# Performance work log

Hardware: AMD Instinct MI355X
Metric: run time of the kernel (lower is better)

## Reference

```python
import jax, jax.numpy as jnp
import numpy as np

N = 100000   # nodes
E = 1600000  # edges
D = 128      # d_model
FF = 512     # dim_feedforward
EPS = 1e-5


def setup_inputs() -> dict:
    key = jax.random.key(0)
    ks = jax.random.split(key, 12)
    x = jax.random.normal(ks[0], (N, D), dtype=jnp.float32)
    edge_index = jax.random.randint(ks[1], (2, E), 0, N, dtype=jnp.int64)
    edge_weight = jax.random.uniform(ks[2], (E,), dtype=jnp.float32)
    sD = 1.0 / np.sqrt(D)
    sFF = 1.0 / np.sqrt(FF)
    W = jax.random.normal(ks[3], (D, D), dtype=jnp.float32) * sD   # GCN weight
    b = jnp.zeros((D,), jnp.float32)                                # GCN bias
    gamma = jnp.ones((D,), jnp.float32)                             # shared batchnorm
    beta = jnp.zeros((D,), jnp.float32)
    W1 = jax.random.normal(ks[4], (D, FF), dtype=jnp.float32) * sD  # MLP lin1
    b1 = jnp.zeros((FF,), jnp.float32)
    W2 = jax.random.normal(ks[5], (FF, D), dtype=jnp.float32) * sFF # MLP lin2
    b2 = jnp.zeros((D,), jnp.float32)
    return {"x": x, "edge_index": edge_index, "edge_weight": edge_weight,
            "W": W, "b": b, "gamma": gamma, "beta": beta,
            "W1": W1, "b1": b1, "W2": W2, "b2": b2}


def gcn_conv(x, edge_index, edge_weight, W, b):
    # GCNConv with add_self_loops=True (self-loop weight 1) and symmetric norm.
    h = x @ W                                   # [N, D]
    src, dst = edge_index[0], edge_index[1]
    deg = jax.ops.segment_sum(edge_weight, dst, num_segments=N) + 1.0
    dinv = jnp.where(deg > 0, jax.lax.rsqrt(deg), 0.0)
    norm = dinv[src] * edge_weight * dinv[dst]  # [E]
    out = jax.ops.segment_sum(norm[:, None] * h[src], dst, num_segments=N)
    out = out + (dinv * dinv)[:, None] * h      # self-loop contribution
    return out + b


def batch_norm(x, gamma, beta):
    # training-mode BatchNorm1d over the node (batch) dimension
    mu = jnp.mean(x, axis=0)
    var = jnp.mean((x - mu) ** 2, axis=0)
    return gamma * (x - mu) * jax.lax.rsqrt(var + EPS) + beta


def reference(x, edge_index, edge_weight, W, b, gamma, beta, W1, b1, W2, b2):
    x1 = batch_norm(x + gcn_conv(x, edge_index, edge_weight, W, b), gamma, beta)
    x2 = jax.nn.relu(x1 @ W1 + b1) @ W2 + b2    # MLP d_model->dim_ff->d_model
    return batch_norm(x1 + x2, gamma, beta)
```

## Files before the change

### kernel.cpp

```cpp
#include <hip/hip_runtime.h>

#define NN 100000
#define EE 1600000
#define DD 128
#define FFD 512
#define EPSV 1e-5f

#define SCB 98

typedef __attribute__((ext_vector_type(8))) short bf16x8;
typedef __attribute__((ext_vector_type(4))) float f32x4;
typedef unsigned long long ull;

__device__ __forceinline__ ushort f2b(float f) {
    uint u = __float_as_uint(f);
    return (ushort)((u + 0x7FFF + ((u >> 16) & 1)) >> 16);
}
__device__ __forceinline__ float b2f(ushort u) {
    return __uint_as_float(((uint)u) << 16);
}


__global__ __launch_bounds__(256) void k_init(ull* pk, float* s1, float* s2) {
    int i = blockIdx.x * 256 + threadIdx.x;
    if (i < NN) pk[i] = 0ULL;
    if (blockIdx.x == 0) { s1[threadIdx.x] = 0.f; s2[threadIdx.x] = 0.f; }
}


__global__ __launch_bounds__(256) void k_edge_deg(const int* __restrict__ ei,
                                                  const float* __restrict__ ew,
                                                  ull* __restrict__ pk,
                                                  int* __restrict__ rank) {
    int e = blockIdx.x * 256 + threadIdx.x;
    if (e < EE) {
        int dst = ei[EE + e];
        uint fx = (uint)(ew[e] * 16777216.0f + 0.5f);
        ull old = atomicAdd(&pk[dst], (1ULL << 32) | (ull)fx);
        rank[e] = (int)(old >> 32);
    }
}


__global__ __launch_bounds__(256) void k_scan_part(const ull* __restrict__ pk,
                                                   int* __restrict__ cnt,
                                                   float* __restrict__ dinv,
                                                   int* __restrict__ bsum) {
    __shared__ int red[4];
    int b = blockIdx.x, t = threadIdx.x;
    int base = b * 1024 + t * 4;
    int s = 0;
#pragma unroll
    for (int j = 0; j < 4; ++j) {
        int i = base + j;
        if (i < NN) {
            ull v = pk[i];
            int c = (int)(v >> 32);
            cnt[i] = c;
            dinv[i] = rsqrtf(1.0f + (float)(uint)(v & 0xFFFFFFFFu) * (1.0f / 16777216.0f));
            s += c;
        }
    }
#pragma unroll
    for (int d = 1; d < 64; d <<= 1) s += __shfl_xor(s, d);
    if ((t & 63) == 0) red[t >> 6] = s;
    __syncthreads();
    if (t == 0) bsum[b] = red[0] + red[1] + red[2] + red[3];
}

__global__ __launch_bounds__(128) void k_scan_base(int* __restrict__ bsum,
                                                   int* __restrict__ bbase,
                                                   int* __restrict__ start) {
    if (threadIdx.x == 0) {
        int run = 0;
        for (int i = 0; i < SCB; ++i) { bbase[i] = run; run += bsum[i]; }
        start[NN] = run;
    }
}

__global__ __launch_bounds__(256) void k_scan_fin(const int* __restrict__ cnt,
                                                  const int* __restrict__ bbase,
                                                  int* __restrict__ start) {
    __shared__ int ts[256];
    int b = blockIdx.x, t = threadIdx.x;
    int base = b * 1024 + t * 4;
    int v[4];
    int s = 0;
#pragma unroll
    for (int j = 0; j < 4; ++j) {
        int i = base + j;
        v[j] = (i < NN) ? cnt[i] : 0;
        s += v[j];
    }
    ts[t] = s;
    __syncthreads();
    for (int d = 1; d < 256; d <<= 1) {
        int add = (t >= d) ? ts[t - d] : 0;
        __syncthreads();
        ts[t] += add;
        __syncthreads();
    }
    int run = bbase[b] + ts[t] - s;
#pragma unroll
    for (int j = 0; j < 4; ++j) {
        int i = base + j;
        if (i < NN) {
            start[i] = run;
            run += v[j];
        }
    }
}


__global__ __launch_bounds__(256) void k_fill(const int* __restrict__ ei,
                                              const float* __restrict__ ew,
                                              const float* __restrict__ dinv,
                                              const int* __restrict__ start,
                                              const int* __restrict__ rank,
                                              uint2* __restrict__ csr) {
    int e = blockIdx.x * 256 + threadIdx.x;
    if (e < EE) {
        int src = ei[e];
        int dst = ei[EE + e];
        float nrm = dinv[src] * ew[e] * dinv[dst];
        int pos = start[dst] + rank[e];
        csr[pos] = make_uint2((uint)src, __float_as_uint(nrm));
    }
}


__global__ __launch_bounds__(256) void k_wcvt(const float* __restrict__ W,
                                              const float* __restrict__ W1,
                                              const float* __restrict__ W2,
                                              ushort* __restrict__ WTb,
                                              ushort* __restrict__ W1Tb,
                                              ushort* __restrict__ W2Tb) {
    int i = blockIdx.x * 256 + threadIdx.x;
    if (i < 16384) {
        int n = i >> 7, k = i & 127;
        WTb[i] = f2b(W[k * 128 + n]);
    } else if (i < 16384 + 65536) {
        int j = i - 16384;
        int f = j >> 7, k = j & 127;
        W1Tb[j] = f2b(W1[k * 512 + f]);
    } else {
        int j = i - 16384 - 65536;
        int jj = j >> 9, f = j & 511;
        W2Tb[j] = f2b(W2[f * 128 + jj]);
    }
}


__global__ __launch_bounds__(256) void k_xb(const float* __restrict__ x,
                                            ushort* __restrict__ xb) {
    long i = (long)blockIdx.x * 256 + threadIdx.x;
    float4 v = ((const float4*)x)[i];
    ushort4 o;
    o.x = f2b(v.x); o.y = f2b(v.y); o.z = f2b(v.z); o.w = f2b(v.w);
    ((ushort4*)xb)[i] = o;
}


__global__ __launch_bounds__(256) void k_gather(const ushort* __restrict__ xb,
                                                const float* __restrict__ dinv,
                                                const int* __restrict__ start,
                                                const uint2* __restrict__ csr,
                                                ushort* __restrict__ aggx) {
    int t = threadIdx.x;
    int wv = t >> 6, l = t & 63;
    const uint* xbu = (const uint*)xb;
    uint* aggu = (uint*)aggx;

    for (int k = 0; k < 8; ++k) {
        int node = blockIdx.x * 32 + wv * 8 + k;
        int e0 = start[node], e1 = start[node + 1];
        float a0 = 0.f, a1 = 0.f;
        int i = e0;
        for (; i + 8 <= e1; i += 8) {
            uint2 rr[8];
            uint hh[8];
#pragma unroll
            for (int u = 0; u < 8; ++u) rr[u] = csr[i + u];
#pragma unroll
            for (int u = 0; u < 8; ++u) hh[u] = xbu[rr[u].x * 64 + l];
#pragma unroll
            for (int u = 0; u < 8; ++u) {
                float n = __uint_as_float(rr[u].y);
                a0 = fmaf(n, b2f((ushort)(hh[u] & 0xFFFF)), a0);
                a1 = fmaf(n, b2f((ushort)(hh[u] >> 16)), a1);
            }
        }
        if (i + 4 <= e1) {
            uint2 rr[4];
            uint hh[4];
#pragma unroll
            for (int u = 0; u < 4; ++u) rr[u] = csr[i + u];
#pragma unroll
            for (int u = 0; u < 4; ++u) hh[u] = xbu[rr[u].x * 64 + l];
#pragma unroll
            for (int u = 0; u < 4; ++u) {
                float n = __uint_as_float(rr[u].y);
                a0 = fmaf(n, b2f((ushort)(hh[u] & 0xFFFF)), a0);
                a1 = fmaf(n, b2f((ushort)(hh[u] >> 16)), a1);
            }
            i += 4;
        }
        for (; i < e1; ++i) {
            uint2 r0 = csr[i];
            uint h0 = xbu[r0.x * 64 + l];
            float n0 = __uint_as_float(r0.y);
            a0 = fmaf(n0, b2f((ushort)(h0 & 0xFFFF)), a0);
            a1 = fmaf(n0, b2f((ushort)(h0 >> 16)), a1);
        }
        float dv = dinv[node];
        float sl = dv * dv;
        uint hs = xbu[node * 64 + l];
        a0 = fmaf(sl, b2f((ushort)(hs & 0xFFFF)), a0);
        a1 = fmaf(sl, b2f((ushort)(hs >> 16)), a1);
        aggu[node * 64 + l] = (uint)f2b(a0) | ((uint)f2b(a1) << 16);
    }
}


__global__ __launch_bounds__(256) void k_conv(const float* __restrict__ x,
                                              const ushort* __restrict__ aggx,
                                              const ushort* __restrict__ WTb,
                                              const float* __restrict__ b,
                                              ushort* __restrict__ yb,
                                              float* __restrict__ stats1) {
    __shared__ __align__(16) ushort xt[64][136];
    __shared__ __align__(16) ushort wt[128][136];
    int t = threadIdx.x;
    int row0 = blockIdx.x * 64;

    for (int i = t; i < 2048; i += 256) {
        int r = i >> 4, c8 = (i & 15) << 3;
        *(uint4*)&wt[r][c8] = ((const uint4*)WTb)[i];
    }
    for (int i = t; i < 1024; i += 256) {
        int r = i >> 4, c8 = (i & 15) << 3;
        int gr = row0 + r;
        uint4 v = make_uint4(0u, 0u, 0u, 0u);
        if (gr < NN) v = ((const uint4*)aggx)[(long)gr * 16 + (i & 15)];
        *(uint4*)&xt[r][c8] = v;
    }
    __syncthreads();

    int wv = t >> 6, l = t & 63;
    int lr = l & 15, lg = l >> 4;
    int rw = wv & 1, jw = wv >> 1;

    f32x4 z4 = {0.f, 0.f, 0.f, 0.f};
    f32x4 acc[4][2];
#pragma unroll
    for (int jt = 0; jt < 4; ++jt)
#pragma unroll
        for (int rt = 0; rt < 2; ++rt) acc[jt][rt] = z4;

#pragma unroll
    for (int ks = 0; ks < 4; ++ks) {
        bf16x8 qR0 = *(const bf16x8*)&xt[rw * 32 + lr][ks * 32 + lg * 8];
        bf16x8 qR1 = *(const bf16x8*)&xt[rw * 32 + 16 + lr][ks * 32 + lg * 8];
#pragma unroll
        for (int jt = 0; jt < 4; ++jt) {
            bf16x8 pW = *(const bf16x8*)&wt[jw * 64 + jt * 16 + lr][ks * 32 + lg * 8];
            acc[jt][0] = __builtin_amdgcn_mfma_f32_16x16x32_bf16(pW, qR0, acc[jt][0], 0, 0, 0);
            acc[jt][1] = __builtin_amdgcn_mfma_f32_16x16x32_bf16(pW, qR1, acc[jt][1], 0, 0, 0);
        }
    }

    float sj[4][4], qj[4][4];
#pragma unroll
    for (int jt = 0; jt < 4; ++jt)
#pragma unroll
        for (int g = 0; g < 4; ++g) { sj[jt][g] = 0.f; qj[jt][g] = 0.f; }

#pragma unroll
    for (int jt = 0; jt < 4; ++jt) {
        int jb = jw * 64 + jt * 16 + lg * 4;
        float4 bv = *(const float4*)&b[jb];
#pragma unroll
        for (int rt = 0; rt < 2; ++rt) {
            int rloc = rw * 32 + rt * 16 + lr;
            int r = row0 + rloc;
            if (r < NN) {
                float4 xv = *(const float4*)&x[(long)r * 128 + jb];
                float z0 = xv.x + acc[jt][rt][0] + bv.x;
                float z1 = xv.y + acc[jt][rt][1] + bv.y;
                float z2 = xv.z + acc[jt][rt][2] + bv.z;
                float z3 = xv.w + acc[jt][rt][3] + bv.w;
                ushort4 o;
                o.x = f2b(z0); o.y = f2b(z1); o.z = f2b(z2); o.w = f2b(z3);
                *(ushort4*)&yb[(long)r * 128 + jb] = o;
                sj[jt][0] += z0; sj[jt][1] += z1; sj[jt][2] += z2; sj[jt][3] += z3;
                qj[jt][0] += z0 * z0; qj[jt][1] += z1 * z1; qj[jt][2] += z2 * z2; qj[jt][3] += z3 * z3;
            }
        }
    }
#pragma unroll
    for (int jt = 0; jt < 4; ++jt)
#pragma unroll
        for (int g = 0; g < 4; ++g) {
#pragma unroll
            for (int d = 1; d < 16; d <<= 1) {
                sj[jt][g] += __shfl_xor(sj[jt][g], d);
                qj[jt][g] += __shfl_xor(qj[jt][g], d);
            }
        }
    __syncthreads();
    float* redS = (float*)&xt[0][0];
    float* redQ = redS + 512;
    if (lr == 0) {
#pragma unroll
        for (int jt = 0; jt < 4; ++jt)
#pragma unroll
            for (int g = 0; g < 4; ++g) {
                int j = jw * 64 + jt * 16 + lg * 4 + g;
                redS[wv * 128 + j] = sj[jt][g];
                redQ[wv * 128 + j] = qj[jt][g];
            }
    }
    __syncthreads();
    if (t < 128) {
        int w0 = (t >> 6) * 2;
        atomicAdd(&stats1[t], redS[w0 * 128 + t] + redS[(w0 + 1) * 128 + t]);
        atomicAdd(&stats1[128 + t], redQ[w0 * 128 + t] + redQ[(w0 + 1) * 128 + t]);
    }
}


__global__ __launch_bounds__(128) void k_bn_fin(const float* __restrict__ stats,
                                                const float* __restrict__ gamma,
                                                const float* __restrict__ beta,
                                                float* __restrict__ ac) {
    int c = threadIdx.x;
    float mu = stats[c] * (1.0f / NN);
    float var = stats[128 + c] * (1.0f / NN) - mu * mu;
    float a = gamma[c] * rsqrtf(var + EPSV);
    ac[c] = a;
    ac[128 + c] = beta[c] - mu * a;
}

__global__ __launch_bounds__(256) void k_affine(float* __restrict__ v,
                                                const float* __restrict__ ac) {
    long i = (long)blockIdx.x * 256 + threadIdx.x;
    int c4i = (int)(i & 31);
    float4 a = ((const float4*)ac)[c4i];
    float4 cc = ((const float4*)(ac + 128))[c4i];
    float4 v4 = ((float4*)v)[i];
    v4.x = a.x * v4.x + cc.x;
    v4.y = a.y * v4.y + cc.y;
    v4.z = a.z * v4.z + cc.z;
    v4.w = a.w * v4.w + cc.w;
    ((float4*)v)[i] = v4;
}


#define SWZ16(row, kb) ((((kb) ^ ((row) & 15)) << 3))

__global__ __launch_bounds__(512, 4) void k_mlp(const ushort* __restrict__ yb,
                                                const float* __restrict__ ac1,
                                                const ushort* __restrict__ W1Tb,
                                                const float* __restrict__ b1,
                                                const ushort* __restrict__ W2Tb,
                                                const float* __restrict__ b2,
                                                float* __restrict__ out,
                                                float* __restrict__ stats2) {
    __shared__ __align__(16) ushort xt[64 * 128];
    __shared__ __align__(16) ushort ht[64 * 128];
    __shared__ __align__(16) ushort wc[128 * 128];
    int t = threadIdx.x;
    int row0 = blockIdx.x * 64;

    for (int i = t; i < 1024; i += 512) {
        int r = i >> 4, kb = i & 15;
        int gr = row0 + r;
        ushort4 y0 = make_ushort4(0, 0, 0, 0), y1 = make_ushort4(0, 0, 0, 0);
        if (gr < NN) {
            long base = (long)gr * 32 + kb * 2;
            y0 = ((const ushort4*)yb)[base];
            y1 = ((const ushort4*)yb)[base + 1];
        }
        float4 a0 = ((const float4*)ac1)[kb * 2];
        float4 a1 = ((const float4*)ac1)[kb * 2 + 1];
        float4 c0 = ((const float4*)(ac1 + 128))[kb * 2];
        float4 c1 = ((const float4*)(ac1 + 128))[kb * 2 + 1];
        ushort4 o0, o1;
        o0.x = f2b(a0.x * b2f(y0.x) + c0.x);
        o0.y = f2b(a0.y * b2f(y0.y) + c0.y);
        o0.z = f2b(a0.z * b2f(y0.z) + c0.z);
        o0.w = f2b(a0.w * b2f(y0.w) + c0.w);
        o1.x = f2b(a1.x * b2f(y1.x) + c1.x);
        o1.y = f2b(a1.y * b2f(y1.y) + c1.y);
        o1.z = f2b(a1.z * b2f(y1.z) + c1.z);
        o1.w = f2b(a1.w * b2f(y1.w) + c1.w);
        ushort* dst = &xt[r * 128 + SWZ16(r, kb)];
        *(ushort4*)dst = o0;
        *(ushort4*)(dst + 4) = o1;
    }

    int wv = t >> 6, l = t & 63;
    int lr = l & 15, lg = l >> 4;
    int rw = wv & 3, jw = wv >> 2;
    int xrow = rw * 16 + lr;

    f32x4 z4 = {0.f, 0.f, 0.f, 0.f};
    f32x4 acc[4];
#pragma unroll
    for (int jt = 0; jt < 4; ++jt) acc[jt] = z4;

    for (int ch = 0; ch < 4; ++ch) {
        __syncthreads();
        for (int i = t; i < 2048; i += 512) {
            int f = i >> 4, kb = i & 15;
            uint4 v = ((const uint4*)W1Tb)[(ch * 128 + f) * 16 + kb];
            *(uint4*)&wc[f * 128 + SWZ16(f, kb)] = v;
        }
        __syncthreads();

        f32x4 hacc[4];
#pragma unroll
        for (int ft = 0; ft < 4; ++ft) hacc[ft] = z4;
#pragma unroll
        for (int ks = 0; ks < 4; ++ks) {
            int kcol = ((ks * 4 + lg) ^ lr) << 3;
            bf16x8 aR = *(const bf16x8*)&xt[xrow * 128 + kcol];
#pragma unroll
            for (int ft = 0; ft < 4; ++ft) {
                int f = jw * 64 + ft * 16 + lr;
                bf16x8 bW = *(const bf16x8*)&wc[f * 128 + kcol];
                hacc[ft] = __builtin_amdgcn_mfma_f32_16x16x32_bf16(aR, bW, hacc[ft], 0, 0, 0);
            }
        }
#pragma unroll
        for (int ft = 0; ft < 4; ++ft) {
            int fcol = jw * 64 + ft * 16 + lr;
            float b1v = b1[ch * 128 + fcol];
            int kbf = fcol >> 3, wi = fcol & 7;
#pragma unroll
            for (int rg = 0; rg < 4; ++rg) {
                int hrow = rw * 16 + lg * 4 + rg;
                ht[hrow * 128 + ((kbf ^ (hrow & 15)) << 3) + wi] =
                    f2b(fmaxf(hacc[ft][rg] + b1v, 0.f));
            }
        }
        __syncthreads();

        for (int i = t; i < 2048; i += 512) {
            int j = i >> 4, kb = i & 15;
            uint4 v = ((const uint4*)W2Tb)[j * 64 + ch * 16 + kb];
            *(uint4*)&wc[j * 128 + SWZ16(j, kb)] = v;
        }
        __syncthreads();

#pragma unroll
        for (int ks = 0; ks < 4; ++ks) {
            int kcol = ((ks * 4 + lg) ^ lr) << 3;
            bf16x8 qR = *(const bf16x8*)&ht[xrow * 128 + kcol];
#pragma unroll
            for (int jt = 0; jt < 4; ++jt) {
                int j = jw * 64 + jt * 16 + lr;
                bf16x8 pW = *(const bf16x8*)&wc[j * 128 + kcol];
                acc[jt] = __builtin_amdgcn_mfma_f32_16x16x32_bf16(pW, qR, acc[jt], 0, 0, 0);
            }
        }
    }

    float sj[4][4], qj[4][4];
    int r = row0 + xrow;
#pragma unroll
    for (int jt = 0; jt < 4; ++jt) {
        int jb = jw * 64 + jt * 16 + lg * 4;
        float4 b2v = *(const float4*)&b2[jb];
        int kbj = jb >> 3, wj = jb & 7;
        ushort4 xv = *(const ushort4*)&xt[xrow * 128 + ((kbj ^ lr) << 3) + wj];
        float z0 = b2f(xv.x) + acc[jt][0] + b2v.x;
        float z1 = b2f(xv.y) + acc[jt][1] + b2v.y;
        float z2 = b2f(xv.z) + acc[jt][2] + b2v.z;
        float z3 = b2f(xv.w) + acc[jt][3] + b2v.w;
        if (r < NN) {
            *(float4*)&out[(long)r * 128 + jb] = make_float4(z0, z1, z2, z3);
            sj[jt][0] = z0; sj[jt][1] = z1; sj[jt][2] = z2; sj[jt][3] = z3;
            qj[jt][0] = z0 * z0; qj[jt][1] = z1 * z1; qj[jt][2] = z2 * z2; qj[jt][3] = z3 * z3;
        } else {
            sj[jt][0] = 0.f; sj[jt][1] = 0.f; sj[jt][2] = 0.f; sj[jt][3] = 0.f;
            qj[jt][0] = 0.f; qj[jt][1] = 0.f; qj[jt][2] = 0.f; qj[jt][3] = 0.f;
        }
    }
#pragma unroll
    for (int jt = 0; jt < 4; ++jt)
#pragma unroll
        for (int g = 0; g < 4; ++g) {
#pragma unroll
            for (int d = 1; d < 16; d <<= 1) {
                sj[jt][g] += __shfl_xor(sj[jt][g], d);
                qj[jt][g] += __shfl_xor(qj[jt][g], d);
            }
        }
    __syncthreads();
    float* redS = (float*)&ht[0];
    float* redQ = redS + 1024;
    if (lr == 0) {
#pragma unroll
        for (int jt = 0; jt < 4; ++jt)
#pragma unroll
            for (int g = 0; g < 4; ++g) {
                int j = jw * 64 + jt * 16 + lg * 4 + g;
                redS[wv * 128 + j] = sj[jt][g];
                redQ[wv * 128 + j] = qj[jt][g];
            }
    }
    __syncthreads();
    if (t < 128) {
        int h = t >> 6;
        float S = redS[(h * 4 + 0) * 128 + t] + redS[(h * 4 + 1) * 128 + t]
                + redS[(h * 4 + 2) * 128 + t] + redS[(h * 4 + 3) * 128 + t];
        float Q = redQ[(h * 4 + 0) * 128 + t] + redQ[(h * 4 + 1) * 128 + t]
                + redQ[(h * 4 + 2) * 128 + t] + redQ[(h * 4 + 3) * 128 + t];
        atomicAdd(&stats2[t], S);
        atomicAdd(&stats2[128 + t], Q);
    }
}


extern "C" void kernel_launch(void* const* d_in, const int* in_sizes, int n_in,
                              void* d_out, int out_size, void* d_ws, size_t ws_size,
                              hipStream_t stream) {
    const float* x     = (const float*)d_in[0];
    const int*   ei    = (const int*)d_in[1];
    const float* ew    = (const float*)d_in[2];
    const float* W     = (const float*)d_in[3];
    const float* b     = (const float*)d_in[4];
    const float* gamma = (const float*)d_in[5];
    const float* beta  = (const float*)d_in[6];
    const float* W1    = (const float*)d_in[7];
    const float* b1    = (const float*)d_in[8];
    const float* W2    = (const float*)d_in[9];
    const float* b2    = (const float*)d_in[10];
    float* out = (float*)d_out;
    float* ws  = (float*)d_ws;

    ull*   pk     = (ull*)ws;
    float* dinv   = ws + 2 * NN;
    float* stats1 = ws + 3 * NN;
    float* ac1    = stats1 + 256;
    float* stats2 = ac1 + 256;
    float* ac2    = stats2 + 256;
    ushort* xb    = (ushort*)(ws + 3 * NN + 1024);
    ushort* WTb   = xb + (long)NN * 128;
    ushort* W1Tb  = WTb + 16384;
    ushort* W2Tb  = W1Tb + 65536;
    float*  fend  = ws + 3 * NN + 1024 + (long)NN * 64 + 73728;
    int*   cnt    = (int*)fend;
    int*   start  = cnt + NN;
    int*   bsum   = start + NN + 1;
    int*   bbase  = bsum + SCB;
    uint2* csr    = (uint2*)(((uintptr_t)(bbase + SCB) + 7) & ~(uintptr_t)7);
    ushort* aggx  = (ushort*)(csr + EE);
    int*   rank   = (int*)aggx;
    ushort* yb    = xb;

    int nb = (NN + 63) / 64;

    k_init<<<(NN + 255) / 256, 256, 0, stream>>>(pk, stats1, stats2);
    k_edge_deg<<<EE / 256, 256, 0, stream>>>(ei, ew, pk, rank);
    k_scan_part<<<SCB, 256, 0, stream>>>(pk, cnt, dinv, bsum);
    k_scan_base<<<1, 128, 0, stream>>>(bsum, bbase, start);
    k_scan_fin<<<SCB, 256, 0, stream>>>(cnt, bbase, start);
    k_fill<<<EE / 256, 256, 0, stream>>>(ei, ew, dinv, start, rank, csr);
    k_wcvt<<<576, 256, 0, stream>>>(W, W1, W2, WTb, W1Tb, W2Tb);
    k_xb<<<(NN * 32) / 256, 256, 0, stream>>>(x, xb);
    k_gather<<<NN / 32, 256, 0, stream>>>(xb, dinv, start, csr, aggx);
    k_conv<<<nb, 256, 0, stream>>>(x, aggx, WTb, b, yb, stats1);
    k_bn_fin<<<1, 128, 0, stream>>>(stats1, gamma, beta, ac1);
    k_mlp<<<nb, 512, 0, stream>>>(yb, ac1, W1Tb, b1, W2Tb, b2, out, stats2);
    k_bn_fin<<<1, 128, 0, stream>>>(stats2, gamma, beta, ac2);
    k_affine<<<(NN * 32) / 256, 256, 0, stream>>>(out, ac2);
}
```

Baseline: 373.6 us.

## Read bf16 residual in conv epilogue and double MLP row tile to 128

The conv epilogue now reads the residual x from the bf16 copy (xb, aliased with yb) instead of fp32 x, halving that read and writing the result back in place. The MLP kernel moves to 1024-thread blocks covering 128 rows, so each staged W1/W2 chunk serves twice as many rows and the block count halves. The risks are lower occupancy from the larger shared memory (about 96 KB per block) and slightly lower residual precision from using bf16 x.

New measurement: 383.9 us. 1.03x slower.

```diff
diff --git a/kernel.cpp b/kernel.cpp
--- a/kernel.cpp
+++ b/kernel.cpp
@@ -222,11 +222,10 @@
 }
 
 
-__global__ __launch_bounds__(256) void k_conv(const float* __restrict__ x,
-                                              const ushort* __restrict__ aggx,
+__global__ __launch_bounds__(256) void k_conv(const ushort* __restrict__ aggx,
                                               const ushort* __restrict__ WTb,
                                               const float* __restrict__ b,
-                                              ushort* __restrict__ yb,
+                                              ushort* xyb,
                                               float* __restrict__ stats1) {
     __shared__ __align__(16) ushort xt[64][136];
     __shared__ __align__(16) ushort wt[128][136];
@@ -284,14 +283,14 @@
             int rloc = rw * 32 + rt * 16 + lr;
             int r = row0 + rloc;
             if (r < NN) {
-                float4 xv = *(const float4*)&x[(long)r * 128 + jb];
-                float z0 = xv.x + acc[jt][rt][0] + bv.x;
-                float z1 = xv.y + acc[jt][rt][1] + bv.y;
-                float z2 = xv.z + acc[jt][rt][2] + bv.z;
-                float z3 = xv.w + acc[jt][rt][3] + bv.w;
+                ushort4 xv = *(const ushort4*)&xyb[(long)r * 128 + jb];
+                float z0 = b2f(xv.x) + acc[jt][rt][0] + bv.x;
+                float z1 = b2f(xv.y) + acc[jt][rt][1] + bv.y;
+                float z2 = b2f(xv.z) + acc[jt][rt][2] + bv.z;
+                float z3 = b2f(xv.w) + acc[jt][rt][3] + bv.w;
                 ushort4 o;
                 o.x = f2b(z0); o.y = f2b(z1); o.z = f2b(z2); o.w = f2b(z3);
-                *(ushort4*)&yb[(long)r * 128 + jb] = o;
+                *(ushort4*)&xyb[(long)r * 128 + jb] = o;
                 sj[jt][0] += z0; sj[jt][1] += z1; sj[jt][2] += z2; sj[jt][3] += z3;
                 qj[jt][0] += z0 * z0; qj[jt][1] += z1 * z1; qj[jt][2] += z2 * z2; qj[jt][3] += z3 * z3;
             }
@@ -358,21 +357,21 @@
 
 #define SWZ16(row, kb) ((((kb) ^ ((row) & 15)) << 3))
 
-__global__ __launch_bounds__(512, 4) void k_mlp(const ushort* __restrict__ yb,
-                                                const float* __restrict__ ac1,
-                                                const ushort* __restrict__ W1Tb,
-                                                const float* __restrict__ b1,
-                                                const ushort* __restrict__ W2Tb,
-                                                const float* __restrict__ b2,
-                                                float* __restrict__ out,
-                                                float* __restrict__ stats2) {
-    __shared__ __align__(16) ushort xt[64 * 128];
-    __shared__ __align__(16) ushort ht[64 * 128];
+__global__ __launch_bounds__(1024) void k_mlp(const ushort* __restrict__ yb,
+                                              const float* __restrict__ ac1,
+                                              const ushort* __restrict__ W1Tb,
+                                              const float* __restrict__ b1,
+                                              const ushort* __restrict__ W2Tb,
+                                              const float* __restrict__ b2,
+                                              float* __restrict__ out,
+                                              float* __restrict__ stats2) {
+    __shared__ __align__(16) ushort xt[128 * 128];
+    __shared__ __align__(16) ushort ht[128 * 128];
     __shared__ __align__(16) ushort wc[128 * 128];
     int t = threadIdx.x;
-    int row0 = blockIdx.x * 64;
-
-    for (int i = t; i < 1024; i += 512) {
+    int row0 = blockIdx.x * 128;
+
+    for (int i = t; i < 2048; i += 1024) {
         int r = i >> 4, kb = i & 15;
         int gr = row0 + r;
         ushort4 y0 = make_ushort4(0, 0, 0, 0), y1 = make_ushort4(0, 0, 0, 0);
@@ -401,7 +400,7 @@
 
     int wv = t >> 6, l = t & 63;
     int lr = l & 15, lg = l >> 4;
-    int rw = wv & 3, jw = wv >> 2;
+    int rw = wv & 7, jw = wv >> 3;
     int xrow = rw * 16 + lr;
 
     f32x4 z4 = {0.f, 0.f, 0.f, 0.f};
@@ -411,7 +410,7 @@
 
     for (int ch = 0; ch < 4; ++ch) {
         __syncthreads();
-        for (int i = t; i < 2048; i += 512) {
+        for (int i = t; i < 2048; i += 1024) {
             int f = i >> 4, kb = i & 15;
             uint4 v = ((const uint4*)W1Tb)[(ch * 128 + f) * 16 + kb];
             *(uint4*)&wc[f * 128 + SWZ16(f, kb)] = v;
@@ -446,7 +445,7 @@
         }
         __syncthreads();
 
-        for (int i = t; i < 2048; i += 512) {
+        for (int i = t; i < 2048; i += 1024) {
             int j = i >> 4, kb = i & 15;
             uint4 v = ((const uint4*)W2Tb)[j * 64 + ch * 16 + kb];
             *(uint4*)&wc[j * 128 + SWZ16(j, kb)] = v;
@@ -499,7 +498,7 @@
         }
     __syncthreads();
     float* redS = (float*)&ht[0];
-    float* redQ = redS + 1024;
+    float* redQ = redS + 2048;
     if (lr == 0) {
 #pragma unroll
         for (int jt = 0; jt < 4; ++jt)
@@ -513,10 +512,12 @@
     __syncthreads();
     if (t < 128) {
         int h = t >> 6;
-        float S = redS[(h * 4 + 0) * 128 + t] + redS[(h * 4 + 1) * 128 + t]
-                + redS[(h * 4 + 2) * 128 + t] + redS[(h * 4 + 3) * 128 + t];
-        float Q = redQ[(h * 4 + 0) * 128 + t] + redQ[(h * 4 + 1) * 128 + t]
-                + redQ[(h * 4 + 2) * 128 + t] + redQ[(h * 4 + 3) * 128 + t];
+        float S = 0.f, Q = 0.f;
+#pragma unroll
+        for (int w = 0; w < 8; ++w) {
+            S += redS[(h * 8 + w) * 128 + t];
+            Q += redQ[(h * 8 + w) * 128 + t];
+        }
         atomicAdd(&stats2[t], S);
         atomicAdd(&stats2[128 + t], Q);
     }
@@ -561,6 +562,7 @@
     ushort* yb    = xb;
 
     int nb = (NN + 63) / 64;
+    int nm = (NN + 127) / 128;
 
     k_init<<<(NN + 255) / 256, 256, 0, stream>>>(pk, stats1, stats2);
     k_edge_deg<<<EE / 256, 256, 0, stream>>>(ei, ew, pk, rank);
@@ -571,9 +573,9 @@
     k_wcvt<<<576, 256, 0, stream>>>(W, W1, W2, WTb, W1Tb, W2Tb);
     k_xb<<<(NN * 32) / 256, 256, 0, stream>>>(x, xb);
     k_gather<<<NN / 32, 256, 0, stream>>>(xb, dinv, start, csr, aggx);
-    k_conv<<<nb, 256, 0, stream>>>(x, aggx, WTb, b, yb, stats1);
+    k_conv<<<nb, 256, 0, stream>>>(aggx, WTb, b, yb, stats1);
     k_bn_fin<<<1, 128, 0, stream>>>(stats1, gamma, beta, ac1);
-    k_mlp<<<nb, 512, 0, stream>>>(yb, ac1, W1Tb, b1, W2Tb, b2, out, stats2);
+    k_mlp<<<nm, 1024, 0, stream>>>(yb, ac1, W1Tb, b1, W2Tb, b2, out, stats2);
     k_bn_fin<<<1, 128, 0, stream>>>(stats2, gamma, beta, ac2);
     k_affine<<<(NN * 32) / 256, 256, 0, stream>>>(out, ac2);
 }
```

## Fuse preprocessing kernels and switch residual/intermediate traffic to bf16

Applied to the files above, without the earlier changes.

Merges the edge-degree atomics, the x-to-bf16 conversion and the weight transpose/convert into one interleaved launch, so the atomic-bound blocks overlap with the streaming conversion blocks. k_conv now reads the residual x from the bf16 copy instead of fp32 and writes its output in place. The MLP output is stored as bf16 into a scratch buffer, and a new affine kernel converts it back to fp32 while applying the final batchnorm, which roughly halves the traffic of that intermediate. The cost is extra bf16 rounding on the residual and on the pre-batchnorm output, which lowers accuracy.

Measured after the change: 360.6 us. -3.5%, faster.

```diff
diff --git a/kernel.cpp b/kernel.cpp
--- a/kernel.cpp
+++ b/kernel.cpp
@@ -7,6 +7,8 @@
 #define EPSV 1e-5f
 
 #define SCB 98
+#define EB 6250
+#define MIXB 18750
 
 typedef __attribute__((ext_vector_type(8))) short bf16x8;
 typedef __attribute__((ext_vector_type(4))) float f32x4;
@@ -28,16 +30,49 @@
 }
 
 
-__global__ __launch_bounds__(256) void k_edge_deg(const int* __restrict__ ei,
-                                                  const float* __restrict__ ew,
-                                                  ull* __restrict__ pk,
-                                                  int* __restrict__ rank) {
-    int e = blockIdx.x * 256 + threadIdx.x;
-    if (e < EE) {
-        int dst = ei[EE + e];
-        uint fx = (uint)(ew[e] * 16777216.0f + 0.5f);
-        ull old = atomicAdd(&pk[dst], (1ULL << 32) | (ull)fx);
-        rank[e] = (int)(old >> 32);
+__global__ __launch_bounds__(256) void k_pre(const int* __restrict__ ei,
+                                             const float* __restrict__ ew,
+                                             ull* __restrict__ pk,
+                                             int* __restrict__ rank,
+                                             const float* __restrict__ x,
+                                             ushort* __restrict__ xb,
+                                             const float* __restrict__ W,
+                                             const float* __restrict__ W1,
+                                             const float* __restrict__ W2,
+                                             ushort* __restrict__ WTb,
+                                             ushort* __restrict__ W1Tb,
+                                             ushort* __restrict__ W2Tb) {
+    int bid = blockIdx.x;
+    int t = threadIdx.x;
+    if (bid < MIXB) {
+        if (bid % 3 == 0) {
+            int e = (bid / 3) * 256 + t;
+            int dst = ei[EE + e];
+            uint fx = (uint)(ew[e] * 16777216.0f + 0.5f);
+            ull old = atomicAdd(&pk[dst], (1ULL << 32) | (ull)fx);
+            rank[e] = (int)(old >> 32);
+        } else {
+            int xbk = bid - bid / 3 - 1;
+            long i = (long)xbk * 256 + t;
+            float4 v = ((const float4*)x)[i];
+            ushort4 o;
+            o.x = f2b(v.x); o.y = f2b(v.y); o.z = f2b(v.z); o.w = f2b(v.w);
+            ((ushort4*)xb)[i] = o;
+        }
+    } else {
+        int i = (bid - MIXB) * 256 + t;
+        if (i < 16384) {
+            int n = i >> 7, k = i & 127;
+            WTb[i] = f2b(W[k * 128 + n]);
+        } else if (i < 16384 + 65536) {
+            int j = i - 16384;
+            int f = j >> 7, k = j & 127;
+            W1Tb[j] = f2b(W1[k * 512 + f]);
+        } else {
+            int j = i - 16384 - 65536;
+            int jj = j >> 9, f = j & 511;
+            W2Tb[j] = f2b(W2[f * 128 + jj]);
+        }
     }
 }
 
@@ -129,38 +164,6 @@
 }
 
 
-__global__ __launch_bounds__(256) void k_wcvt(const float* __restrict__ W,
-                                              const float* __restrict__ W1,
-                                              const float* __restrict__ W2,
-                                              ushort* __restrict__ WTb,
-                                              ushort* __restrict__ W1Tb,
-                                              ushort* __restrict__ W2Tb) {
-    int i = blockIdx.x * 256 + threadIdx.x;
-    if (i < 16384) {
-        int n = i >> 7, k = i & 127;
-        WTb[i] = f2b(W[k * 128 + n]);
-    } else if (i < 16384 + 65536) {
-        int j = i - 16384;
-        int f = j >> 7, k = j & 127;
-        W1Tb[j] = f2b(W1[k * 512 + f]);
-    } else {
-        int j = i - 16384 - 65536;
-        int jj = j >> 9, f = j & 511;
-        W2Tb[j] = f2b(W2[f * 128 + jj]);
-    }
-}
-
-
-__global__ __launch_bounds__(256) void k_xb(const float* __restrict__ x,
-                                            ushort* __restrict__ xb) {
-    long i = (long)blockIdx.x * 256 + threadIdx.x;
-    float4 v = ((const float4*)x)[i];
-    ushort4 o;
-    o.x = f2b(v.x); o.y = f2b(v.y); o.z = f2b(v.z); o.w = f2b(v.w);
-    ((ushort4*)xb)[i] = o;
-}
-
-
 __global__ __launch_bounds__(256) void k_gather(const ushort* __restrict__ xb,
                                                 const float* __restrict__ dinv,
                                                 const int* __restrict__ start,
@@ -222,11 +225,10 @@
 }
 
 
-__global__ __launch_bounds__(256) void k_conv(const float* __restrict__ x,
-                                              const ushort* __restrict__ aggx,
+__global__ __launch_bounds__(256) void k_conv(const ushort* __restrict__ aggx,
                                               const ushort* __restrict__ WTb,
                                               const float* __restrict__ b,
-                                              ushort* __restrict__ yb,
+                                              ushort* xyb,
                                               float* __restrict__ stats1) {
     __shared__ __align__(16) ushort xt[64][136];
     __shared__ __align__(16) ushort wt[128][136];
@@ -284,14 +286,14 @@
             int rloc = rw * 32 + rt * 16 + lr;
             int r = row0 + rloc;
             if (r < NN) {
-                float4 xv = *(const float4*)&x[(long)r * 128 + jb];
-                float z0 = xv.x + acc[jt][rt][0] + bv.x;
-                float z1 = xv.y + acc[jt][rt][1] + bv.y;
-                float z2 = xv.z + acc[jt][rt][2] + bv.z;
-                float z3 = xv.w + acc[jt][rt][3] + bv.w;
+                ushort4 xv = *(const ushort4*)&xyb[(long)r * 128 + jb];
+                float z0 = b2f(xv.x) + acc[jt][rt][0] + bv.x;
+                float z1 = b2f(xv.y) + acc[jt][rt][1] + bv.y;
+                float z2 = b2f(xv.z) + acc[jt][rt][2] + bv.z;
+                float z3 = b2f(xv.w) + acc[jt][rt][3] + bv.w;
                 ushort4 o;
                 o.x = f2b(z0); o.y = f2b(z1); o.z = f2b(z2); o.w = f2b(z3);
-                *(ushort4*)&yb[(long)r * 128 + jb] = o;
+                *(ushort4*)&xyb[(long)r * 128 + jb] = o;
                 sj[jt][0] += z0; sj[jt][1] += z1; sj[jt][2] += z2; sj[jt][3] += z3;
                 qj[jt][0] += z0 * z0; qj[jt][1] += z1 * z1; qj[jt][2] += z2 * z2; qj[jt][3] += z3 * z3;
             }
@@ -341,18 +343,21 @@
     ac[128 + c] = beta[c] - mu * a;
 }
 
-__global__ __launch_bounds__(256) void k_affine(float* __restrict__ v,
-                                                const float* __restrict__ ac) {
+
+__global__ __launch_bounds__(256) void k_affine2(const ushort* __restrict__ zb,
+                                                 const float* __restrict__ ac,
+                                                 float* __restrict__ out) {
     long i = (long)blockIdx.x * 256 + threadIdx.x;
     int c4i = (int)(i & 31);
     float4 a = ((const float4*)ac)[c4i];
     float4 cc = ((const float4*)(ac + 128))[c4i];
-    float4 v4 = ((float4*)v)[i];
-    v4.x = a.x * v4.x + cc.x;
-    v4.y = a.y * v4.y + cc.y;
-    v4.z = a.z * v4.z + cc.z;
-    v4.w = a.w * v4.w + cc.w;
-    ((float4*)v)[i] = v4;
+    ushort4 zv = ((const ushort4*)zb)[i];
+    float4 o;
+    o.x = a.x * b2f(zv.x) + cc.x;
+    o.y = a.y * b2f(zv.y) + cc.y;
+    o.z = a.z * b2f(zv.z) + cc.z;
+    o.w = a.w * b2f(zv.w) + cc.w;
+    ((float4*)out)[i] = o;
 }
 
 
@@ -364,7 +369,7 @@
                                                 const float* __restrict__ b1,
                                                 const ushort* __restrict__ W2Tb,
                                                 const float* __restrict__ b2,
-                                                float* __restrict__ out,
+                                                ushort* __restrict__ zb,
                                                 float* __restrict__ stats2) {
     __shared__ __align__(16) ushort xt[64 * 128];
     __shared__ __align__(16) ushort ht[64 * 128];
@@ -479,7 +484,9 @@
         float z2 = b2f(xv.z) + acc[jt][2] + b2v.z;
         float z3 = b2f(xv.w) + acc[jt][3] + b2v.w;
         if (r < NN) {
-            *(float4*)&out[(long)r * 128 + jb] = make_float4(z0, z1, z2, z3);
+            ushort4 o;
+            o.x = f2b(z0); o.y = f2b(z1); o.z = f2b(z2); o.w = f2b(z3);
+            *(ushort4*)&zb[(long)r * 128 + jb] = o;
             sj[jt][0] = z0; sj[jt][1] = z1; sj[jt][2] = z2; sj[jt][3] = z3;
             qj[jt][0] = z0 * z0; qj[jt][1] = z1 * z1; qj[jt][2] = z2 * z2; qj[jt][3] = z3 * z3;
         } else {
@@ -559,21 +566,20 @@
     ushort* aggx  = (ushort*)(csr + EE);
     int*   rank   = (int*)aggx;
     ushort* yb    = xb;
+    ushort* zb    = aggx;
 
     int nb = (NN + 63) / 64;
 
     k_init<<<(NN + 255) / 256, 256, 0, stream>>>(pk, stats1, stats2);
-    k_edge_deg<<<EE / 256, 256, 0, stream>>>(ei, ew, pk, rank);
+    k_pre<<<MIXB + 576, 256, 0, stream>>>(ei, ew, pk, rank, x, xb, W, W1, W2, WTb, W1Tb, W2Tb);
     k_scan_part<<<SCB, 256, 0, stream>>>(pk, cnt, dinv, bsum);
     k_scan_base<<<1, 128, 0, stream>>>(bsum, bbase, start);
     k_scan_fin<<<SCB, 256, 0, stream>>>(cnt, bbase, start);
     k_fill<<<EE / 256, 256, 0, stream>>>(ei, ew, dinv, start, rank, csr);
-    k_wcvt<<<576, 256, 0, stream>>>(W, W1, W2, WTb, W1Tb, W2Tb);
-    k_xb<<<(NN * 32) / 256, 256, 0, stream>>>(x, xb);
     k_gather<<<NN / 32, 256, 0, stream>>>(xb, dinv, start, csr, aggx);
-    k_conv<<<nb, 256, 0, stream>>>(x, aggx, WTb, b, yb, stats1);
+    k_conv<<<nb, 256, 0, stream>>>(aggx, WTb, b, yb, stats1);
     k_bn_fin<<<1, 128, 0, stream>>>(stats1, gamma, beta, ac1);
-    k_mlp<<<nb, 512, 0, stream>>>(yb, ac1, W1Tb, b1, W2Tb, b2, out, stats2);
+    k_mlp<<<nb, 512, 0, stream>>>(yb, ac1, W1Tb, b1, W2Tb, b2, zb, stats2);
     k_bn_fin<<<1, 128, 0, stream>>>(stats2, gamma, beta, ac2);
-    k_affine<<<(NN * 32) / 256, 256, 0, stream>>>(out, ac2);
-}
+    k_affine2<<<(NN * 32) / 256, 256, 0, stream>>>(zb, ac2, out);
+}
```
